# Performance work log

Hardware: AMD Instinct MI355X
Metric: run time of the kernel (lower is better)

The kernel has to match this reference:

```python
import jax, jax.numpy as jnp
import numpy as np

ALPHA = 0.2  # LeakyReLU negative slope
NEG_INF = -9e15

def leaky_relu(x):
    return jnp.where(x >= 0, x, ALPHA * x)

def setup_inputs() -> dict:
    key = jax.random.key(0)
    ks = jax.random.split(key, 7)
    B, N, D = 8, 1024, 256
    R = 12
    return {
        "h0": jax.random.normal(ks[0], (B, N, D), jnp.float32),
        "h1": jax.random.normal(ks[1], (B, N, D), jnp.float32),
        "multi_adj": jax.random.randint(ks[2], (R, B, N, N), 0, 2, jnp.int32),
        "adj": jax.random.randint(ks[3], (B, N, N), 0, 2, jnp.int32),
        "W": jax.random.normal(ks[4], (D, D), jnp.float32) * 0.05,
        "a": jax.random.normal(ks[5], (2 * D,), jnp.float32) * 0.05,
        "A_rel": jax.random.normal(ks[6], (R, 2 * D), jnp.float32) * 0.05,
    }

def reference(h0, h1, multi_adj, adj, W, a, A_rel):
    D = W.shape[1]
    Wh0 = jnp.einsum('bnd,de->bne', h0, W)  # [B,N0,D]
    Wh1 = jnp.einsum('bnd,de->bne', h1, W)  # [B,N1,D]
    # a_input @ v decomposes into outer-sum of per-node projections
    s0 = Wh0 @ a[:D]                         # [B,N0]
    s1 = Wh1 @ a[D:]                         # [B,N1]
    e = leaky_relu(s0[:, :, None] + s1[:, None, :])  # [B,N0,N1]
    attention = jnp.where(adj > 0, e, NEG_INF)
    # 12 relation score maps, fused: r0[r,b,i] + r1[r,b,j]
    r0 = jnp.einsum('bnd,rd->rbn', Wh0, A_rel[:, :D])  # [R,B,N0]
    r1 = jnp.einsum('bnd,rd->rbn', Wh1, A_rel[:, D:])  # [R,B,N1]
    e_rel = leaky_relu(r0[:, :, :, None] + r1[:, :, None, :])  # [R,B,N0,N1]
    rel_sum = jnp.where(multi_adj > 0, e_rel, 0.0).sum(axis=0)  # [B,N0,N1]
    # note: original softmax is over dim=1 (source-node axis N0)
    att = jax.nn.softmax(attention + 0.01 * rel_sum, axis=1)
    # dropout omitted (eval mode / deterministic baseline)
    h_prime = jnp.einsum('bij,bjd->bid', att, Wh1)
    return jax.nn.elu(h_prime)  # concat=True
```

## Files before the change

### kernel.cpp

```cpp
#include <hip/hip_runtime.h>
#include <hip/hip_bf16.h>

#define BB 8
#define NN 1024
#define DD 256
#define RR 12
#define BN (BB * NN)
#define ICH 8
#define CCH (NN / ICH)

typedef __attribute__((ext_vector_type(8))) short short8v;
typedef __attribute__((ext_vector_type(4))) float f32x4;

static __device__ __forceinline__ ushort f2bf(float f) {
  union { float f; uint u; } v; v.f = f;
  uint r = v.u + 0x7FFF + ((v.u >> 16) & 1);
  return (ushort)(r >> 16);
}
static __device__ __forceinline__ uint pack2(float a, float b) {
  return (uint)f2bf(a) | ((uint)f2bf(b) << 16);
}

__global__ __launch_bounds__(256) void k_prepW(const float* __restrict__ W,
                                               ushort* __restrict__ WTb) {
  __shared__ float Ls[64][65];
  int k0 = blockIdx.x * 64, d0 = blockIdx.y * 64;
  int tid = threadIdx.x;
  int rr = tid >> 4, c = (tid & 15) * 4;
#pragma unroll
  for (int p = 0; p < 4; ++p) {
    int row = p * 16 + rr;
    float4 v = *(const float4*)&W[(k0 + row) * DD + d0 + c];
    Ls[row][c] = v.x; Ls[row][c + 1] = v.y; Ls[row][c + 2] = v.z; Ls[row][c + 3] = v.w;
  }
  __syncthreads();
  int r2 = tid >> 3, cc = (tid & 7) * 8;
#pragma unroll
  for (int p = 0; p < 2; ++p) {
    int d = p * 32 + r2;
    uint4 q;
    q.x = pack2(Ls[cc + 0][d], Ls[cc + 1][d]);
    q.y = pack2(Ls[cc + 2][d], Ls[cc + 3][d]);
    q.z = pack2(Ls[cc + 4][d], Ls[cc + 5][d]);
    q.w = pack2(Ls[cc + 6][d], Ls[cc + 7][d]);
    *(uint4*)&WTb[(d0 + d) * DD + k0 + cc] = q;
  }
}

__global__ __launch_bounds__(256) void k_transWh(const float* __restrict__ Wh,
                                                 ushort* __restrict__ WhT) {
  __shared__ float Ls[64][65];
  int z = blockIdx.z;
  int d0 = blockIdx.x * 64, i0 = blockIdx.y * 64;
  int tid = threadIdx.x;
  int rr = tid >> 4, c = (tid & 15) * 4;
#pragma unroll
  for (int p = 0; p < 4; ++p) {
    int row = p * 16 + rr;
    float4 v = *(const float4*)&Wh[(long)(z * NN + i0 + row) * DD + d0 + c];
    Ls[row][c] = v.x; Ls[row][c + 1] = v.y; Ls[row][c + 2] = v.z; Ls[row][c + 3] = v.w;
  }
  __syncthreads();
  int r2 = tid >> 3, cc = (tid & 7) * 8;
#pragma unroll
  for (int p = 0; p < 2; ++p) {
    int d = p * 32 + r2;
    uint4 q;
    q.x = pack2(Ls[cc + 0][d], Ls[cc + 1][d]);
    q.y = pack2(Ls[cc + 2][d], Ls[cc + 3][d]);
    q.z = pack2(Ls[cc + 4][d], Ls[cc + 5][d]);
    q.w = pack2(Ls[cc + 6][d], Ls[cc + 7][d]);
    *(uint4*)&WhT[(long)z * DD * NN + (long)(d0 + d) * NN + i0 + cc] = q;
  }
}

template <int K, bool SM, bool ELU, bool SPLITA>
__global__ __launch_bounds__(256) void k_mm(const float* __restrict__ A0,
                                            const float* __restrict__ A1,
                                            const ushort* __restrict__ BT,
                                            const float* __restrict__ mf,
                                            const float* __restrict__ li,
                                            float* __restrict__ C,
                                            long sAz, long sBz, long sCz) {
  __shared__ uint4 AswQ[64 * 8];
  __shared__ uint4 BswQ[128 * 8];
  int z = blockIdx.z;
  const float* Ab = SPLITA ? (z ? A1 : A0) : A0 + (long)z * sAz;
  const ushort* Bb = BT + (long)z * sBz;
  float* Cb = C + (long)z * sCz;
  const float* mfb = mf + (long)z * NN;
  const float* lib = li + (long)z * NN;
  int i0 = blockIdx.y * 64;
  int n0 = blockIdx.x * 128;
  int tid = threadIdx.x;
  int r = tid >> 3, cs = tid & 7;
  int lane = tid & 63, wid = tid >> 6;
  int wm = wid >> 1, wn = wid & 1;
  int lr = lane & 15, g = lane >> 4;
  f32x4 acc[2][4] = {};
  for (int k0 = 0; k0 < K; k0 += 64) {
#pragma unroll
    for (int p = 0; p < 2; ++p) {
      int row = p * 32 + r;
      const float* src = Ab + (long)(i0 + row) * K + k0 + cs * 8;
      float4 v0 = *(const float4*)src;
      float4 v1 = *(const float4*)(src + 4);
      if (SM) {
        const float* mp = mfb + k0 + cs * 8;
        const float* lp = lib + k0 + cs * 8;
        float4 m0 = *(const float4*)mp, m1 = *(const float4*)(mp + 4);
        float4 l0 = *(const float4*)lp, l1 = *(const float4*)(lp + 4);
        v0.x = __expf(v0.x - m0.x) * l0.x;
        v0.y = __expf(v0.y - m0.y) * l0.y;
        v0.z = __expf(v0.z - m0.z) * l0.z;
        v0.w = __expf(v0.w - m0.w) * l0.w;
        v1.x = __expf(v1.x - m1.x) * l1.x;
        v1.y = __expf(v1.y - m1.y) * l1.y;
        v1.z = __expf(v1.z - m1.z) * l1.z;
        v1.w = __expf(v1.w - m1.w) * l1.w;
      }
      uint4 q;
      q.x = pack2(v0.x, v0.y);
      q.y = pack2(v0.z, v0.w);
      q.z = pack2(v1.x, v1.y);
      q.w = pack2(v1.z, v1.w);
      AswQ[row * 8 + (cs ^ (row & 7))] = q;
    }
#pragma unroll
    for (int p = 0; p < 4; ++p) {
      int row = p * 32 + r;
      uint4 q = *(const uint4*)(Bb + (long)(n0 + row) * K + k0 + cs * 8);
      BswQ[row * 8 + (cs ^ (row & 7))] = q;
    }
    __syncthreads();
#pragma unroll
    for (int ks = 0; ks < 2; ++ks) {
      short8v af[2], bfr[4];
      int slot = ks * 4 + g;
#pragma unroll
      for (int mi = 0; mi < 2; ++mi) {
        int row = wm * 32 + mi * 16 + lr;
        af[mi] = *reinterpret_cast<const short8v*>(&AswQ[row * 8 + (slot ^ (row & 7))]);
      }
#pragma unroll
      for (int ni = 0; ni < 4; ++ni) {
        int row = wn * 64 + ni * 16 + lr;
        bfr[ni] = *reinterpret_cast<const short8v*>(&BswQ[row * 8 + (slot ^ (row & 7))]);
      }
#pragma unroll
      for (int mi = 0; mi < 2; ++mi)
#pragma unroll
        for (int ni = 0; ni < 4; ++ni)
          acc[mi][ni] = __builtin_amdgcn_mfma_f32_16x16x32_bf16(af[mi], bfr[ni], acc[mi][ni], 0, 0, 0);
    }
    __syncthreads();
  }
#pragma unroll
  for (int mi = 0; mi < 2; ++mi)
#pragma unroll
    for (int ni = 0; ni < 4; ++ni) {
#pragma unroll
      for (int q = 0; q < 4; ++q) {
        int row = i0 + wm * 32 + mi * 16 + g * 4 + q;
        int col = n0 + wn * 64 + ni * 16 + lr;
        float x = acc[mi][ni][q];
        if (ELU) x = x > 0.f ? x : expm1f(x);
        Cb[(long)row * DD + col] = x;
      }
    }
}

__global__ __launch_bounds__(256) void k_proj(const float* __restrict__ Wh0,
                                              const float* __restrict__ Wh1,
                                              const float* __restrict__ a,
                                              const float* __restrict__ A_rel,
                                              float* __restrict__ s0, float* __restrict__ s1,
                                              float* __restrict__ r0, float* __restrict__ r1) {
  int wid = (blockIdx.x * 256 + threadIdx.x) >> 6;
  int lane = threadIdx.x & 63;
  int mat = wid >> 13;
  int row = wid & (BN - 1);
  const float* Wh = mat ? Wh1 : Wh0;
  float4 h4 = *(const float4*)&Wh[row * DD + lane * 4];
  {
    float4 v4 = *(const float4*)&a[mat * DD + lane * 4];
    float p = h4.x * v4.x + h4.y * v4.y + h4.z * v4.z + h4.w * v4.w;
#pragma unroll
    for (int off = 32; off; off >>= 1) p += __shfl_xor(p, off);
    if (lane == 0) (mat ? s1 : s0)[row] = p;
  }
  for (int r = 0; r < RR; ++r) {
    float4 w4 = *(const float4*)&A_rel[r * 2 * DD + mat * DD + lane * 4];
    float q = h4.x * w4.x + h4.y * w4.y + h4.z * w4.z + h4.w * w4.w;
#pragma unroll
    for (int off = 32; off; off >>= 1) q += __shfl_xor(q, off);
    if (lane == 0) (mat ? r1 : r0)[r * BN + row] = q;
  }
}

__global__ __launch_bounds__(256) void k_scores(const int* __restrict__ madj,
                                                const int* __restrict__ adj,
                                                const float* __restrict__ s0,
                                                const float* __restrict__ s1,
                                                const float* __restrict__ r0,
                                                const float* __restrict__ r1,
                                                float* __restrict__ S,
                                                float* __restrict__ pm,
                                                float* __restrict__ pl) {
  int b = blockIdx.x, c = blockIdx.y;
  int tid = threadIdx.x;
  int j4 = tid * 4;
  int i0 = c * ICH;
  __shared__ float s0c[ICH];
  __shared__ float r0c[RR][ICH];
  if (tid < (RR + 1) * ICH) {
    int v = tid / ICH, i = tid % ICH;
    float x = (v == 0) ? s0[b * NN + i0 + i] : r0[(v - 1) * BN + b * NN + i0 + i];
    if (v == 0) s0c[i] = x; else r0c[v - 1][i] = x;
  }
  __syncthreads();
  float4 s14 = *(const float4*)&s1[b * NN + j4];
  float rel[ICH][4] = {};
  for (int r = 0; r < RR; ++r) {
    float4 r1v = *(const float4*)&r1[r * BN + b * NN + j4];
#pragma unroll
    for (int i = 0; i < ICH; ++i) {
      int4 mv = *(const int4*)&madj[(((long)r * BB + b) * NN + i0 + i) * NN + j4];
      float r0v = r0c[r][i];
      float t0 = r0v + r1v.x; t0 = t0 >= 0.f ? t0 : 0.2f * t0;
      float t1 = r0v + r1v.y; t1 = t1 >= 0.f ? t1 : 0.2f * t1;
      float t2 = r0v + r1v.z; t2 = t2 >= 0.f ? t2 : 0.2f * t2;
      float t3 = r0v + r1v.w; t3 = t3 >= 0.f ? t3 : 0.2f * t3;
      if (mv.x > 0) rel[i][0] += t0;
      if (mv.y > 0) rel[i][1] += t1;
      if (mv.z > 0) rel[i][2] += t2;
      if (mv.w > 0) rel[i][3] += t3;
    }
  }
  float m0 = -3.0e38f, m1 = -3.0e38f, m2 = -3.0e38f, m3 = -3.0e38f;
  float l0 = 0.f, l1 = 0.f, l2 = 0.f, l3 = 0.f;
#pragma unroll
  for (int i = 0; i < ICH; ++i) {
    int4 av = *(const int4*)&adj[((long)b * NN + i0 + i) * NN + j4];
    float s0v = s0c[i];
    float4 sc;
    {
      float e = s0v + s14.x; e = e >= 0.f ? e : 0.2f * e;
      sc.x = (av.x > 0 ? e : -9e15f) + 0.01f * rel[i][0];
    }
    {
      float e = s0v + s14.y; e = e >= 0.f ? e : 0.2f * e;
      sc.y = (av.y > 0 ? e : -9e15f) + 0.01f * rel[i][1];
    }
    {
      float e = s0v + s14.z; e = e >= 0.f ? e : 0.2f * e;
      sc.z = (av.z > 0 ? e : -9e15f) + 0.01f * rel[i][2];
    }
    {
      float e = s0v + s14.w; e = e >= 0.f ? e : 0.2f * e;
      sc.w = (av.w > 0 ? e : -9e15f) + 0.01f * rel[i][3];
    }
    *(float4*)&S[((long)b * NN + i0 + i) * NN + j4] = sc;
    float nm;
    nm = fmaxf(m0, sc.x); l0 = l0 * __expf(m0 - nm) + __expf(sc.x - nm); m0 = nm;
    nm = fmaxf(m1, sc.y); l1 = l1 * __expf(m1 - nm) + __expf(sc.y - nm); m1 = nm;
    nm = fmaxf(m2, sc.z); l2 = l2 * __expf(m2 - nm) + __expf(sc.z - nm); m2 = nm;
    nm = fmaxf(m3, sc.w); l3 = l3 * __expf(m3 - nm) + __expf(sc.w - nm); m3 = nm;
  }
  *(float4*)&pm[(long)c * BN + b * NN + j4] = make_float4(m0, m1, m2, m3);
  *(float4*)&pl[(long)c * BN + b * NN + j4] = make_float4(l0, l1, l2, l3);
}

__global__ __launch_bounds__(256) void k_combine(const float* __restrict__ pm,
                                                 const float* __restrict__ pl,
                                                 float* __restrict__ mf,
                                                 float* __restrict__ li) {
  int col = blockIdx.x * 256 + threadIdx.x;
  float m = -3.0e38f;
#pragma unroll 8
  for (int c = 0; c < CCH; ++c) m = fmaxf(m, pm[(long)c * BN + col]);
  float l = 0.f;
#pragma unroll 8
  for (int c = 0; c < CCH; ++c) l += pl[(long)c * BN + col] * __expf(pm[(long)c * BN + col] - m);
  mf[col] = m;
  li[col] = 1.0f / l;
}

extern "C" void kernel_launch(void* const* d_in, const int* in_sizes, int n_in,
                              void* d_out, int out_size, void* d_ws, size_t ws_size,
                              hipStream_t stream) {
  const float* h0 = (const float*)d_in[0];
  const float* h1 = (const float*)d_in[1];
  const int* madj = (const int*)d_in[2];
  const int* adj = (const int*)d_in[3];
  const float* W = (const float*)d_in[4];
  const float* a = (const float*)d_in[5];
  const float* A_rel = (const float*)d_in[6];
  float* out = (float*)d_out;

  float* ws = (float*)d_ws;
  float* Wh0 = ws;
  float* Wh1 = Wh0 + (size_t)BN * DD;
  float* S = Wh1 + (size_t)BN * DD;
  float* s0 = S + (size_t)BB * NN * NN;
  float* s1 = s0 + BN;
  float* r0 = s1 + BN;
  float* r1 = r0 + RR * BN;
  float* pm = r1 + RR * BN;
  float* pl = pm + (size_t)CCH * BN;
  float* mf = pl + (size_t)CCH * BN;
  float* li = mf + BN;
  ushort* WTb = (ushort*)(li + BN);
  ushort* WhbT = WTb + DD * DD;

  k_prepW<<<dim3(4, 4), 256, 0, stream>>>(W, WTb);
  k_mm<DD, false, false, true><<<dim3(2, BN / 64, 2), 256, 0, stream>>>(
      h0, h1, WTb, mf, li, Wh0, 0, 0, (long)BN * DD);
  k_transWh<<<dim3(4, 16, 8), 256, 0, stream>>>(Wh1, WhbT);
  k_proj<<<(2 * BN) / 4, 256, 0, stream>>>(Wh0, Wh1, a, A_rel, s0, s1, r0, r1);
  k_scores<<<dim3(BB, CCH), 256, 0, stream>>>(madj, adj, s0, s1, r0, r1, S, pm, pl);
  k_combine<<<BN / 256, 256, 0, stream>>>(pm, pl, mf, li);
  k_mm<NN, true, true, false><<<dim3(2, NN / 64, BB), 256, 0, stream>>>(
      S, S, WhbT, mf, li, out, (long)NN * NN, (long)DD * NN, (long)NN * DD);
}
```

Measured before the change: 200.8 us.

## Fold projections into W, drop Wh0 GEMM, merge kernels, retile AV GEMM

Precomputes W·a and W·A_rel vectors so the s/r projections are taken directly from h0/h1, which removes the Wh0 GEMM entirely. The Wh1 GEMM and projection share one launch, the Wh1 transpose runs alongside the score kernel, and the combine step is parallelised across chunk segments with a tree reduction. The final attention·V GEMM uses 32-row tiles for more blocks. The aim is fewer launches and less redundant GEMM work. The trade-off is projections computed from fp32 h rather than from bf16-rounded Wh, plus smaller MFMA tiles with less reuse per block.

```diff
diff --git a/kernel.cpp b/kernel.cpp
--- a/kernel.cpp
+++ b/kernel.cpp
@@ -21,269 +21,356 @@
   return (uint)f2bf(a) | ((uint)f2bf(b) << 16);
 }
 
-__global__ __launch_bounds__(256) void k_prepW(const float* __restrict__ W,
-                                               ushort* __restrict__ WTb) {
+__global__ __launch_bounds__(256) void k_prep(const float* __restrict__ W,
+                                              const float* __restrict__ a,
+                                              const float* __restrict__ A_rel,
+                                              ushort* __restrict__ WTb,
+                                              float* __restrict__ Vt) {
   __shared__ float Ls[64][65];
-  int k0 = blockIdx.x * 64, d0 = blockIdx.y * 64;
-  int tid = threadIdx.x;
-  int rr = tid >> 4, c = (tid & 15) * 4;
-#pragma unroll
-  for (int p = 0; p < 4; ++p) {
-    int row = p * 16 + rr;
-    float4 v = *(const float4*)&W[(k0 + row) * DD + d0 + c];
-    Ls[row][c] = v.x; Ls[row][c + 1] = v.y; Ls[row][c + 2] = v.z; Ls[row][c + 3] = v.w;
-  }
-  __syncthreads();
-  int r2 = tid >> 3, cc = (tid & 7) * 8;
-#pragma unroll
-  for (int p = 0; p < 2; ++p) {
-    int d = p * 32 + r2;
-    uint4 q;
-    q.x = pack2(Ls[cc + 0][d], Ls[cc + 1][d]);
-    q.y = pack2(Ls[cc + 2][d], Ls[cc + 3][d]);
-    q.z = pack2(Ls[cc + 4][d], Ls[cc + 5][d]);
-    q.w = pack2(Ls[cc + 6][d], Ls[cc + 7][d]);
-    *(uint4*)&WTb[(d0 + d) * DD + k0 + cc] = q;
-  }
-}
-
-__global__ __launch_bounds__(256) void k_transWh(const float* __restrict__ Wh,
-                                                 ushort* __restrict__ WhT) {
-  __shared__ float Ls[64][65];
-  int z = blockIdx.z;
-  int d0 = blockIdx.x * 64, i0 = blockIdx.y * 64;
-  int tid = threadIdx.x;
-  int rr = tid >> 4, c = (tid & 15) * 4;
-#pragma unroll
-  for (int p = 0; p < 4; ++p) {
-    int row = p * 16 + rr;
-    float4 v = *(const float4*)&Wh[(long)(z * NN + i0 + row) * DD + d0 + c];
-    Ls[row][c] = v.x; Ls[row][c + 1] = v.y; Ls[row][c + 2] = v.z; Ls[row][c + 3] = v.w;
-  }
-  __syncthreads();
-  int r2 = tid >> 3, cc = (tid & 7) * 8;
-#pragma unroll
-  for (int p = 0; p < 2; ++p) {
-    int d = p * 32 + r2;
-    uint4 q;
-    q.x = pack2(Ls[cc + 0][d], Ls[cc + 1][d]);
-    q.y = pack2(Ls[cc + 2][d], Ls[cc + 3][d]);
-    q.z = pack2(Ls[cc + 4][d], Ls[cc + 5][d]);
-    q.w = pack2(Ls[cc + 6][d], Ls[cc + 7][d]);
-    *(uint4*)&WhT[(long)z * DD * NN + (long)(d0 + d) * NN + i0 + cc] = q;
-  }
-}
-
-template <int K, bool SM, bool ELU, bool SPLITA>
-__global__ __launch_bounds__(256) void k_mm(const float* __restrict__ A0,
-                                            const float* __restrict__ A1,
-                                            const ushort* __restrict__ BT,
-                                            const float* __restrict__ mf,
-                                            const float* __restrict__ li,
-                                            float* __restrict__ C,
-                                            long sAz, long sBz, long sCz) {
+  int blk = blockIdx.x, tid = threadIdx.x;
+  if (blk < 16) {
+    int k0 = (blk & 3) * 64, d0 = (blk >> 2) * 64;
+    int rr = tid >> 4, c = (tid & 15) * 4;
+#pragma unroll
+    for (int p = 0; p < 4; ++p) {
+      int row = p * 16 + rr;
+      float4 v = *(const float4*)&W[(k0 + row) * DD + d0 + c];
+      Ls[row][c] = v.x; Ls[row][c + 1] = v.y; Ls[row][c + 2] = v.z; Ls[row][c + 3] = v.w;
+    }
+    __syncthreads();
+    int r2 = tid >> 3, cc = (tid & 7) * 8;
+#pragma unroll
+    for (int p = 0; p < 2; ++p) {
+      int d = p * 32 + r2;
+      uint4 q;
+      q.x = pack2(Ls[cc + 0][d], Ls[cc + 1][d]);
+      q.y = pack2(Ls[cc + 2][d], Ls[cc + 3][d]);
+      q.z = pack2(Ls[cc + 4][d], Ls[cc + 5][d]);
+      q.w = pack2(Ls[cc + 6][d], Ls[cc + 7][d]);
+      *(uint4*)&WTb[(d0 + d) * DD + k0 + cc] = q;
+    }
+  } else {
+    int idx = blk - 16;
+    int half = idx >= 26 ? 1 : 0;
+    int c = idx - half * 26;
+    if (c >= 13) return;
+    int k = tid;
+    float acc = 0.f;
+    for (int d4 = 0; d4 < DD / 4; ++d4) {
+      float4 w4 = *(const float4*)&W[k * DD + d4 * 4];
+      float4 x4;
+      if (c == 0) x4 = *(const float4*)&a[half * DD + d4 * 4];
+      else        x4 = *(const float4*)&A_rel[(c - 1) * 2 * DD + half * DD + d4 * 4];
+      acc += w4.x * x4.x + w4.y * x4.y + w4.z * x4.z + w4.w * x4.w;
+    }
+    Vt[(half * 13 + c) * DD + k] = acc;
+  }
+}
+
+__global__ __launch_bounds__(256) void k_wh_proj(const float* __restrict__ h0,
+                                                 const float* __restrict__ h1,
+                                                 const ushort* __restrict__ WTb,
+                                                 const float* __restrict__ Vt,
+                                                 float* __restrict__ Wh1,
+                                                 float* __restrict__ s0, float* __restrict__ s1,
+                                                 float* __restrict__ r0, float* __restrict__ r1) {
   __shared__ uint4 AswQ[64 * 8];
   __shared__ uint4 BswQ[128 * 8];
-  int z = blockIdx.z;
-  const float* Ab = SPLITA ? (z ? A1 : A0) : A0 + (long)z * sAz;
-  const ushort* Bb = BT + (long)z * sBz;
-  float* Cb = C + (long)z * sCz;
-  const float* mfb = mf + (long)z * NN;
-  const float* lib = li + (long)z * NN;
-  int i0 = blockIdx.y * 64;
-  int n0 = blockIdx.x * 128;
-  int tid = threadIdx.x;
-  int r = tid >> 3, cs = tid & 7;
-  int lane = tid & 63, wid = tid >> 6;
-  int wm = wid >> 1, wn = wid & 1;
-  int lr = lane & 15, g = lane >> 4;
-  f32x4 acc[2][4] = {};
-  for (int k0 = 0; k0 < K; k0 += 64) {
+  int blk = blockIdx.x, tid = threadIdx.x;
+  if (blk < 256) {
+    int n0 = (blk & 1) * 128, i0 = (blk >> 1) * 64;
+    int r = tid >> 3, cs = tid & 7;
+    int lane = tid & 63, wid = tid >> 6;
+    int wm = wid >> 1, wn = wid & 1;
+    int lr = lane & 15, g = lane >> 4;
+    f32x4 acc[2][4] = {};
+    for (int k0 = 0; k0 < DD; k0 += 64) {
+#pragma unroll
+      for (int p = 0; p < 2; ++p) {
+        int row = p * 32 + r;
+        const float* src = h1 + (long)(i0 + row) * DD + k0 + cs * 8;
+        float4 v0 = *(const float4*)src;
+        float4 v1 = *(const float4*)(src + 4);
+        uint4 q;
+        q.x = pack2(v0.x, v0.y); q.y = pack2(v0.z, v0.w);
+        q.z = pack2(v1.x, v1.y); q.w = pack2(v1.z, v1.w);
+        AswQ[row * 8 + (cs ^ (row & 7))] = q;
+      }
+#pragma unroll
+      for (int p = 0; p < 4; ++p) {
+        int row = p * 32 + r;
+        uint4 q = *(const uint4*)(WTb + (long)(n0 + row) * DD + k0 + cs * 8);
+        BswQ[row * 8 + (cs ^ (row & 7))] = q;
+      }
+      __syncthreads();
+#pragma unroll
+      for (int ks = 0; ks < 2; ++ks) {
+        short8v af[2], bfr[4];
+        int slot = ks * 4 + g;
+#pragma unroll
+        for (int mi = 0; mi < 2; ++mi) {
+          int row = wm * 32 + mi * 16 + lr;
+          af[mi] = *reinterpret_cast<const short8v*>(&AswQ[row * 8 + (slot ^ (row & 7))]);
+        }
+#pragma unroll
+        for (int ni = 0; ni < 4; ++ni) {
+          int row = wn * 64 + ni * 16 + lr;
+          bfr[ni] = *reinterpret_cast<const short8v*>(&BswQ[row * 8 + (slot ^ (row & 7))]);
+        }
+#pragma unroll
+        for (int mi = 0; mi < 2; ++mi)
+#pragma unroll
+          for (int ni = 0; ni < 4; ++ni)
+            acc[mi][ni] = __builtin_amdgcn_mfma_f32_16x16x32_bf16(af[mi], bfr[ni], acc[mi][ni], 0, 0, 0);
+      }
+      __syncthreads();
+    }
+#pragma unroll
+    for (int mi = 0; mi < 2; ++mi)
+#pragma unroll
+      for (int ni = 0; ni < 4; ++ni)
+#pragma unroll
+        for (int q = 0; q < 4; ++q) {
+          int row = i0 + wm * 32 + mi * 16 + g * 4 + q;
+          int col = n0 + wn * 64 + ni * 16 + lr;
+          Wh1[(long)row * DD + col] = acc[mi][ni][q];
+        }
+  } else {
+    int w = ((blk - 256) << 2) + (tid >> 6);
+    int lane = tid & 63;
+    for (int it = 0; it < 16; ++it) {
+      int row = w + (it << 10);
+      int mat = row >> 13, rr = row & (BN - 1);
+      const float* h = mat ? h1 : h0;
+      float4 h4 = *(const float4*)&h[(long)rr * DD + lane * 4];
+#pragma unroll
+      for (int c = 0; c < 13; ++c) {
+        float4 v4 = *(const float4*)&Vt[(mat * 13 + c) * DD + lane * 4];
+        float p = h4.x * v4.x + h4.y * v4.y + h4.z * v4.z + h4.w * v4.w;
+#pragma unroll
+        for (int off = 32; off; off >>= 1) p += __shfl_xor(p, off);
+        if (lane == 0) {
+          if (c == 0) (mat ? s1 : s0)[rr] = p;
+          else (mat ? r1 : r0)[(c - 1) * BN + rr] = p;
+        }
+      }
+    }
+  }
+}
+
+__global__ __launch_bounds__(256) void k_trans_scores(const float* __restrict__ Wh1,
+                                                      ushort* __restrict__ WhT,
+                                                      const int* __restrict__ madj,
+                                                      const int* __restrict__ adj,
+                                                      const float* __restrict__ s0,
+                                                      const float* __restrict__ s1,
+                                                      const float* __restrict__ r0,
+                                                      const float* __restrict__ r1,
+                                                      float* __restrict__ S,
+                                                      float* __restrict__ pm,
+                                                      float* __restrict__ pl) {
+  union Sm {
+    float Ls[64][65];
+    struct { float s0c[ICH]; float r0c[RR][ICH]; } sc;
+  };
+  __shared__ Sm sm;
+  int blk = blockIdx.x, tid = threadIdx.x;
+  if (blk < 1024) {
+    int b = blk & 7, c = blk >> 3;
+    int j4 = tid * 4;
+    int i0 = c * ICH;
+    if (tid < (RR + 1) * ICH) {
+      int v = tid / ICH, i = tid % ICH;
+      float x = (v == 0) ? s0[b * NN + i0 + i] : r0[(v - 1) * BN + b * NN + i0 + i];
+      if (v == 0) sm.sc.s0c[i] = x; else sm.sc.r0c[v - 1][i] = x;
+    }
+    __syncthreads();
+    float4 s14 = *(const float4*)&s1[b * NN + j4];
+    float rel[ICH][4] = {};
+    for (int r = 0; r < RR; ++r) {
+      float4 r1v = *(const float4*)&r1[r * BN + b * NN + j4];
+#pragma unroll
+      for (int i = 0; i < ICH; ++i) {
+        int4 mv = *(const int4*)&madj[(((long)r * BB + b) * NN + i0 + i) * NN + j4];
+        float r0v = sm.sc.r0c[r][i];
+        float t0 = r0v + r1v.x; t0 = t0 >= 0.f ? t0 : 0.2f * t0;
+        float t1 = r0v + r1v.y; t1 = t1 >= 0.f ? t1 : 0.2f * t1;
+        float t2 = r0v + r1v.z; t2 = t2 >= 0.f ? t2 : 0.2f * t2;
+        float t3 = r0v + r1v.w; t3 = t3 >= 0.f ? t3 : 0.2f * t3;
+        if (mv.x > 0) rel[i][0] += t0;
+        if (mv.y > 0) rel[i][1] += t1;
+        if (mv.z > 0) rel[i][2] += t2;
+        if (mv.w > 0) rel[i][3] += t3;
+      }
+    }
+    float m0 = -3.0e38f, m1 = -3.0e38f, m2 = -3.0e38f, m3 = -3.0e38f;
+    float l0 = 0.f, l1 = 0.f, l2 = 0.f, l3 = 0.f;
+#pragma unroll
+    for (int i = 0; i < ICH; ++i) {
+      int4 av = *(const int4*)&adj[((long)b * NN + i0 + i) * NN + j4];
+      float s0v = sm.sc.s0c[i];
+      float4 sc;
+      { float e = s0v + s14.x; e = e >= 0.f ? e : 0.2f * e;
+        sc.x = (av.x > 0 ? e : -9e15f) + 0.01f * rel[i][0]; }
+      { float e = s0v + s14.y; e = e >= 0.f ? e : 0.2f * e;
+        sc.y = (av.y > 0 ? e : -9e15f) + 0.01f * rel[i][1]; }
+      { float e = s0v + s14.z; e = e >= 0.f ? e : 0.2f * e;
+        sc.z = (av.z > 0 ? e : -9e15f) + 0.01f * rel[i][2]; }
+      { float e = s0v + s14.w; e = e >= 0.f ? e : 0.2f * e;
+        sc.w = (av.w > 0 ? e : -9e15f) + 0.01f * rel[i][3]; }
+      *(float4*)&S[((long)b * NN + i0 + i) * NN + j4] = sc;
+      float nm;
+      nm = fmaxf(m0, sc.x); l0 = l0 * __expf(m0 - nm) + __expf(sc.x - nm); m0 = nm;
+      nm = fmaxf(m1, sc.y); l1 = l1 * __expf(m1 - nm) + __expf(sc.y - nm); m1 = nm;
+      nm = fmaxf(m2, sc.z); l2 = l2 * __expf(m2 - nm) + __expf(sc.z - nm); m2 = nm;
+      nm = fmaxf(m3, sc.w); l3 = l3 * __expf(m3 - nm) + __expf(sc.w - nm); m3 = nm;
+    }
+    *(float4*)&pm[(long)c * BN + b * NN + j4] = make_float4(m0, m1, m2, m3);
+    *(float4*)&pl[(long)c * BN + b * NN + j4] = make_float4(l0, l1, l2, l3);
+  } else {
+    int t = blk - 1024;
+    int d0 = (t & 3) * 64, i0 = ((t >> 2) & 15) * 64, z = t >> 6;
+    int rr = tid >> 4, c = (tid & 15) * 4;
+#pragma unroll
+    for (int p = 0; p < 4; ++p) {
+      int row = p * 16 + rr;
+      float4 v = *(const float4*)&Wh1[(long)(z * NN + i0 + row) * DD + d0 + c];
+      sm.Ls[row][c] = v.x; sm.Ls[row][c + 1] = v.y;
+      sm.Ls[row][c + 2] = v.z; sm.Ls[row][c + 3] = v.w;
+    }
+    __syncthreads();
+    int r2 = tid >> 3, cc = (tid & 7) * 8;
 #pragma unroll
     for (int p = 0; p < 2; ++p) {
-      int row = p * 32 + r;
-      const float* src = Ab + (long)(i0 + row) * K + k0 + cs * 8;
-      float4 v0 = *(const float4*)src;
-      float4 v1 = *(const float4*)(src + 4);
-      if (SM) {
-        const float* mp = mfb + k0 + cs * 8;
-        const float* lp = lib + k0 + cs * 8;
-        float4 m0 = *(const float4*)mp, m1 = *(const float4*)(mp + 4);
-        float4 l0 = *(const float4*)lp, l1 = *(const float4*)(lp + 4);
-        v0.x = __expf(v0.x - m0.x) * l0.x;
-        v0.y = __expf(v0.y - m0.y) * l0.y;
-        v0.z = __expf(v0.z - m0.z) * l0.z;
-        v0.w = __expf(v0.w - m0.w) * l0.w;
-        v1.x = __expf(v1.x - m1.x) * l1.x;
-        v1.y = __expf(v1.y - m1.y) * l1.y;
-        v1.z = __expf(v1.z - m1.z) * l1.z;
-        v1.w = __expf(v1.w - m1.w) * l1.w;
-      }
+      int d = p * 32 + r2;
       uint4 q;
-      q.x = pack2(v0.x, v0.y);
-      q.y = pack2(v0.z, v0.w);
-      q.z = pack2(v1.x, v1.y);
-      q.w = pack2(v1.z, v1.w);
-      AswQ[row * 8 + (cs ^ (row & 7))] = q;
-    }
-#pragma unroll
-    for (int p = 0; p < 4; ++p) {
-      int row = p * 32 + r;
-      uint4 q = *(const uint4*)(Bb + (long)(n0 + row) * K + k0 + cs * 8);
-      BswQ[row * 8 + (cs ^ (row & 7))] = q;
-    }
-    __syncthreads();
-#pragma unroll
-    for (int ks = 0; ks < 2; ++ks) {
-      short8v af[2], bfr[4];
-      int slot = ks * 4 + g;
-#pragma unroll
-      for (int mi = 0; mi < 2; ++mi) {
-        int row = wm * 32 + mi * 16 + lr;
-        af[mi] = *reinterpret_cast<const short8v*>(&AswQ[row * 8 + (slot ^ (row & 7))]);
-      }
-#pragma unroll
-      for (int ni = 0; ni < 4; ++ni) {
-        int row = wn * 64 + ni * 16 + lr;
-        bfr[ni] = *reinterpret_cast<const short8v*>(&BswQ[row * 8 + (slot ^ (row & 7))]);
-      }
-#pragma unroll
-      for (int mi = 0; mi < 2; ++mi)
-#pragma unroll
-        for (int ni = 0; ni < 4; ++ni)
-          acc[mi][ni] = __builtin_amdgcn_mfma_f32_16x16x32_bf16(af[mi], bfr[ni], acc[mi][ni], 0, 0, 0);
-    }
-    __syncthreads();
-  }
-#pragma unroll
-  for (int mi = 0; mi < 2; ++mi)
-#pragma unroll
-    for (int ni = 0; ni < 4; ++ni) {
-#pragma unroll
-      for (int q = 0; q < 4; ++q) {
-        int row = i0 + wm * 32 + mi * 16 + g * 4 + q;
-        int col = n0 + wn * 64 + ni * 16 + lr;
-        float x = acc[mi][ni][q];
-        if (ELU) x = x > 0.f ? x : expm1f(x);
-        Cb[(long)row * DD + col] = x;
-      }
-    }
-}
-
-__global__ __launch_bounds__(256) void k_proj(const float* __restrict__ Wh0,
-                                              const float* __restrict__ Wh1,
-                                              const float* __restrict__ a,
-                                              const float* __restrict__ A_rel,
-                                              float* __restrict__ s0, float* __restrict__ s1,
-                                              float* __restrict__ r0, float* __restrict__ r1) {
-  int wid = (blockIdx.x * 256 + threadIdx.x) >> 6;
-  int lane = threadIdx.x & 63;
-  int mat = wid >> 13;
-  int row = wid & (BN - 1);
-  const float* Wh = mat ? Wh1 : Wh0;
-  float4 h4 = *(const float4*)&Wh[row * DD + lane * 4];
-  {
-    float4 v4 = *(const float4*)&a[mat * DD + lane * 4];
-    float p = h4.x * v4.x + h4.y * v4.y + h4.z * v4.z + h4.w * v4.w;
-#pragma unroll
-    for (int off = 32; off; off >>= 1) p += __shfl_xor(p, off);
-    if (lane == 0) (mat ? s1 : s0)[row] = p;
-  }
-  for (int r = 0; r < RR; ++r) {
-    float4 w4 = *(const float4*)&A_rel[r * 2 * DD + mat * DD + lane * 4];
-    float q = h4.x * w4.x + h4.y * w4.y + h4.z * w4.z + h4.w * w4.w;
-#pragma unroll
-    for (int off = 32; off; off >>= 1) q += __shfl_xor(q, off);
-    if (lane == 0) (mat ? r1 : r0)[r * BN + row] = q;
-  }
-}
-
-__global__ __launch_bounds__(256) void k_scores(const int* __restrict__ madj,
-                                                const int* __restrict__ adj,
-                                                const float* __restrict__ s0,
-                                                const float* __restrict__ s1,
-                                                const float* __restrict__ r0,
-                                                const float* __restrict__ r1,
-                                                float* __restrict__ S,
-                                                float* __restrict__ pm,
-                                                float* __restrict__ pl) {
-  int b = blockIdx.x, c = blockIdx.y;
-  int tid = threadIdx.x;
-  int j4 = tid * 4;
-  int i0 = c * ICH;
-  __shared__ float s0c[ICH];
-  __shared__ float r0c[RR][ICH];
-  if (tid < (RR + 1) * ICH) {
-    int v = tid / ICH, i = tid % ICH;
-    float x = (v == 0) ? s0[b * NN + i0 + i] : r0[(v - 1) * BN + b * NN + i0 + i];
-    if (v == 0) s0c[i] = x; else r0c[v - 1][i] = x;
-  }
-  __syncthreads();
-  float4 s14 = *(const float4*)&s1[b * NN + j4];
-  float rel[ICH][4] = {};
-  for (int r = 0; r < RR; ++r) {
-    float4 r1v = *(const float4*)&r1[r * BN + b * NN + j4];
-#pragma unroll
-    for (int i = 0; i < ICH; ++i) {
-      int4 mv = *(const int4*)&madj[(((long)r * BB + b) * NN + i0 + i) * NN + j4];
-      float r0v = r0c[r][i];
-      float t0 = r0v + r1v.x; t0 = t0 >= 0.f ? t0 : 0.2f * t0;
-      float t1 = r0v + r1v.y; t1 = t1 >= 0.f ? t1 : 0.2f * t1;
-      float t2 = r0v + r1v.z; t2 = t2 >= 0.f ? t2 : 0.2f * t2;
-      float t3 = r0v + r1v.w; t3 = t3 >= 0.f ? t3 : 0.2f * t3;
-      if (mv.x > 0) rel[i][0] += t0;
-      if (mv.y > 0) rel[i][1] += t1;
-      if (mv.z > 0) rel[i][2] += t2;
-      if (mv.w > 0) rel[i][3] += t3;
-    }
-  }
-  float m0 = -3.0e38f, m1 = -3.0e38f, m2 = -3.0e38f, m3 = -3.0e38f;
-  float l0 = 0.f, l1 = 0.f, l2 = 0.f, l3 = 0.f;
-#pragma unroll
-  for (int i = 0; i < ICH; ++i) {
-    int4 av = *(const int4*)&adj[((long)b * NN + i0 + i) * NN + j4];
-    float s0v = s0c[i];
-    float4 sc;
-    {
-      float e = s0v + s14.x; e = e >= 0.f ? e : 0.2f * e;
-      sc.x = (av.x > 0 ? e : -9e15f) + 0.01f * rel[i][0];
-    }
-    {
-      float e = s0v + s14.y; e = e >= 0.f ? e : 0.2f * e;
-      sc.y = (av.y > 0 ? e : -9e15f) + 0.01f * rel[i][1];
-    }
-    {
-      float e = s0v + s14.z; e = e >= 0.f ? e : 0.2f * e;
-      sc.z = (av.z > 0 ? e : -9e15f) + 0.01f * rel[i][2];
-    }
-    {
-      float e = s0v + s14.w; e = e >= 0.f ? e : 0.2f * e;
-      sc.w = (av.w > 0 ? e : -9e15f) + 0.01f * rel[i][3];
-    }
-    *(float4*)&S[((long)b * NN + i0 + i) * NN + j4] = sc;
-    float nm;
-    nm = fmaxf(m0, sc.x); l0 = l0 * __expf(m0 - nm) + __expf(sc.x - nm); m0 = nm;
-    nm = fmaxf(m1, sc.y); l1 = l1 * __expf(m1 - nm) + __expf(sc.y - nm); m1 = nm;
-    nm = fmaxf(m2, sc.z); l2 = l2 * __expf(m2 - nm) + __expf(sc.z - nm); m2 = nm;
-    nm = fmaxf(m3, sc.w); l3 = l3 * __expf(m3 - nm) + __expf(sc.w - nm); m3 = nm;
-  }
-  *(float4*)&pm[(long)c * BN + b * NN + j4] = make_float4(m0, m1, m2, m3);
-  *(float4*)&pl[(long)c * BN + b * NN + j4] = make_float4(l0, l1, l2, l3);
+      q.x = pack2(sm.Ls[cc + 0][d], sm.Ls[cc + 1][d]);
+      q.y = pack2(sm.Ls[cc + 2][d], sm.Ls[cc + 3][d]);
+      q.z = pack2(sm.Ls[cc + 4][d], sm.Ls[cc + 5][d]);
+      q.w = pack2(sm.Ls[cc + 6][d], sm.Ls[cc + 7][d]);
+      *(uint4*)&WhT[(long)z * DD * NN + (long)(d0 + d) * NN + i0 + cc] = q;
+    }
+  }
 }
 
 __global__ __launch_bounds__(256) void k_combine(const float* __restrict__ pm,
                                                  const float* __restrict__ pl,
                                                  float* __restrict__ mf,
                                                  float* __restrict__ li) {
-  int col = blockIdx.x * 256 + threadIdx.x;
-  float m = -3.0e38f;
-#pragma unroll 8
-  for (int c = 0; c < CCH; ++c) m = fmaxf(m, pm[(long)c * BN + col]);
-  float l = 0.f;
-#pragma unroll 8
-  for (int c = 0; c < CCH; ++c) l += pl[(long)c * BN + col] * __expf(pm[(long)c * BN + col] - m);
-  mf[col] = m;
-  li[col] = 1.0f / l;
+  __shared__ float sm_m[256], sm_l[256];
+  int tid = threadIdx.x;
+  int col_l = tid & 15, seg = tid >> 4;
+  int col = blockIdx.x * 16 + col_l;
+  float m = -3.0e38f, l = 0.f;
+#pragma unroll
+  for (int q = 0; q < 8; ++q) {
+    int c = seg * 8 + q;
+    float mc = pm[(long)c * BN + col];
+    float lc = pl[(long)c * BN + col];
+    float nm = fmaxf(m, mc);
+    l = l * __expf(m - nm) + lc * __expf(mc - nm);
+    m = nm;
+  }
+  sm_m[tid] = m; sm_l[tid] = l;
+  __syncthreads();
+  for (int s = 8; s; s >>= 1) {
+    if (seg < s) {
+      float ma = sm_m[tid], la = sm_l[tid];
+      float mb = sm_m[tid + s * 16], lb = sm_l[tid + s * 16];
+      float nm = fmaxf(ma, mb);
+      sm_m[tid] = nm;
+      sm_l[tid] = la * __expf(ma - nm) + lb * __expf(mb - nm);
+    }
+    __syncthreads();
+  }
+  if (seg == 0) {
+    mf[col] = sm_m[tid];
+    li[col] = 1.0f / sm_l[tid];
+  }
+}
+
+__global__ __launch_bounds__(256) void k_av(const float* __restrict__ S,
+                                            const float* __restrict__ mf,
+                                            const float* __restrict__ li,
+                                            const ushort* __restrict__ WhT,
+                                            float* __restrict__ out) {
+  __shared__ uint4 AswQ[32 * 8];
+  __shared__ uint4 BswQ[128 * 8];
+  int b = blockIdx.z;
+  int i0 = blockIdx.y * 32;
+  int n0 = blockIdx.x * 128;
+  const float* Sb = S + (long)b * NN * NN;
+  const ushort* Bb = WhT + (long)b * DD * NN;
+  const float* mfb = mf + (long)b * NN;
+  const float* lib = li + (long)b * NN;
+  int tid = threadIdx.x;
+  int r = tid >> 3, cs = tid & 7;
+  int lane = tid & 63, wid = tid >> 6;
+  int lr = lane & 15, g = lane >> 4;
+  f32x4 acc[2][2] = {};
+  for (int k0 = 0; k0 < NN; k0 += 64) {
+    {
+      const float* src = Sb + (long)(i0 + r) * NN + k0 + cs * 8;
+      float4 v0 = *(const float4*)src;
+      float4 v1 = *(const float4*)(src + 4);
+      const float* mp = mfb + k0 + cs * 8;
+      const float* lp = lib + k0 + cs * 8;
+      float4 m0 = *(const float4*)mp, m1 = *(const float4*)(mp + 4);
+      float4 l0 = *(const float4*)lp, l1 = *(const float4*)(lp + 4);
+      v0.x = __expf(v0.x - m0.x) * l0.x;
+      v0.y = __expf(v0.y - m0.y) * l0.y;
+      v0.z = __expf(v0.z - m0.z) * l0.z;
+      v0.w = __expf(v0.w - m0.w) * l0.w;
+      v1.x = __expf(v1.x - m1.x) * l1.x;
+      v1.y = __expf(v1.y - m1.y) * l1.y;
+      v1.z = __expf(v1.z - m1.z) * l1.z;
+      v1.w = __expf(v1.w - m1.w) * l1.w;
+      uint4 q;
+      q.x = pack2(v0.x, v0.y); q.y = pack2(v0.z, v0.w);
+      q.z = pack2(v1.x, v1.y); q.w = pack2(v1.z, v1.w);
+      AswQ[r * 8 + (cs ^ (r & 7))] = q;
+    }
+#pragma unroll
+    for (int p = 0; p < 4; ++p) {
+      int row = p * 32 + r;
+      uint4 q = *(const uint4*)(Bb + (long)(n0 + row) * NN + k0 + cs * 8);
+      BswQ[row * 8 + (cs ^ (row & 7))] = q;
+    }
+    __syncthreads();
+#pragma unroll
+    for (int ks = 0; ks < 2; ++ks) {
+      short8v af[2], bfr[2];
+      int slot = ks * 4 + g;
+#pragma unroll
+      for (int mi = 0; mi < 2; ++mi) {
+        int row = mi * 16 + lr;
+        af[mi] = *reinterpret_cast<const short8v*>(&AswQ[row * 8 + (slot ^ (row & 7))]);
+      }
+#pragma unroll
+      for (int ni = 0; ni < 2; ++ni) {
+        int row = wid * 32 + ni * 16 + lr;
+        bfr[ni] = *reinterpret_cast<const short8v*>(&BswQ[row * 8 + (slot ^ (row & 7))]);
+      }
+#pragma unroll
+      for (int mi = 0; mi < 2; ++mi)
+#pragma unroll
+        for (int ni = 0; ni < 2; ++ni)
+          acc[mi][ni] = __builtin_amdgcn_mfma_f32_16x16x32_bf16(af[mi], bfr[ni], acc[mi][ni], 0, 0, 0);
+    }
+    __syncthreads();
+  }
+#pragma unroll
+  for (int mi = 0; mi < 2; ++mi)
+#pragma unroll
+    for (int ni = 0; ni < 2; ++ni)
+#pragma unroll
+      for (int q = 0; q < 4; ++q) {
+        int row = i0 + mi * 16 + g * 4 + q;
+        int col = n0 + wid * 32 + ni * 16 + lr;
+        float x = acc[mi][ni][q];
+        x = x > 0.f ? x : expm1f(x);
+        out[((long)b * NN + row) * DD + col] = x;
+      }
 }
 
 extern "C" void kernel_launch(void* const* d_in, const int* in_sizes, int n_in,
@@ -299,8 +386,7 @@
   float* out = (float*)d_out;
 
   float* ws = (float*)d_ws;
-  float* Wh0 = ws;
-  float* Wh1 = Wh0 + (size_t)BN * DD;
+  float* Wh1 = ws;
   float* S = Wh1 + (size_t)BN * DD;
   float* s0 = S + (size_t)BB * NN * NN;
   float* s1 = s0 + BN;
@@ -310,16 +396,13 @@
   float* pl = pm + (size_t)CCH * BN;
   float* mf = pl + (size_t)CCH * BN;
   float* li = mf + BN;
-  ushort* WTb = (ushort*)(li + BN);
+  float* Vt = li + BN;
+  ushort* WTb = (ushort*)(Vt + 26 * DD);
   ushort* WhbT = WTb + DD * DD;
 
-  k_prepW<<<dim3(4, 4), 256, 0, stream>>>(W, WTb);
-  k_mm<DD, false, false, true><<<dim3(2, BN / 64, 2), 256, 0, stream>>>(
-      h0, h1, WTb, mf, li, Wh0, 0, 0, (long)BN * DD);
-  k_transWh<<<dim3(4, 16, 8), 256, 0, stream>>>(Wh1, WhbT);
-  k_proj<<<(2 * BN) / 4, 256, 0, stream>>>(Wh0, Wh1, a, A_rel, s0, s1, r0, r1);
-  k_scores<<<dim3(BB, CCH), 256, 0, stream>>>(madj, adj, s0, s1, r0, r1, S, pm, pl);
-  k_combine<<<BN / 256, 256, 0, stream>>>(pm, pl, mf, li);
-  k_mm<NN, true, true, false><<<dim3(2, NN / 64, BB), 256, 0, stream>>>(
-      S, S, WhbT, mf, li, out, (long)NN * NN, (long)DD * NN, (long)NN * DD);
-}
+  k_prep<<<68, 256, 0, stream>>>(W, a, A_rel, WTb, Vt);
+  k_wh_proj<<<512, 256, 0, stream>>>(h0, h1, WTb, Vt, Wh1, s0, s1, r0, r1);
+  k_trans_scores<<<1536, 256, 0, stream>>>(Wh1, WhbT, madj, adj, s0, s1, r0, r1, S, pm, pl);
+  k_combine<<<512, 256, 0, stream>>>(pm, pl, mf, li);
+  k_av<<<dim3(2, NN / 32, BB), 256, 0, stream>>>(S, mf, li, WhbT, out);
+}
```

New measurement: 239.7 us. 19.4% more time.
